# Kernel tuning notes

Hardware: AMD Instinct MI355X
Metric: run time of the kernel (lower is better)

## Reference

```python
import jax, jax.numpy as jnp
import numpy as np

NUM_HEADS = 32
NUM_KV_HEADS = 8
HEAD_DIM = 128
WINDOW = 512
NUM_META = 4


def _swa_sink_mask(S):
    # allowed = causal & (within sliding window OR sink/meta token)
    i = jnp.arange(S)[:, None]   # q_idx
    j = jnp.arange(S)[None, :]   # kv_idx
    return (i >= j) & (((i - j) <= WINDOW) | (j < NUM_META))


def setup_inputs() -> dict:
    key = jax.random.key(0)
    k1, k2, k3 = jax.random.split(key, 3)
    B, S = 1, 2048
    return {
        "query_states": jax.random.normal(k1, (B, S, NUM_HEADS * HEAD_DIM), dtype=jnp.float32),
        "key_states": jax.random.normal(k2, (B, S, NUM_KV_HEADS * HEAD_DIM), dtype=jnp.float32),
        "value_states": jax.random.normal(k3, (B, S, NUM_KV_HEADS * HEAD_DIM), dtype=jnp.float32),
    }


def reference(query_states, key_states, value_states):
    B, S, _ = query_states.shape
    n_rep = NUM_HEADS // NUM_KV_HEADS
    # [B, H, S, D]
    q = query_states.reshape(B, S, NUM_HEADS, HEAD_DIM).transpose(0, 2, 1, 3)
    k = key_states.reshape(B, S, NUM_KV_HEADS, HEAD_DIM).transpose(0, 2, 1, 3)
    v = value_states.reshape(B, S, NUM_KV_HEADS, HEAD_DIM).transpose(0, 2, 1, 3)
    # repeat_kv: interleaved repeat along head dim (GQA)
    k = jnp.repeat(k, n_rep, axis=1)
    v = jnp.repeat(v, n_rep, axis=1)

    scale = 1.0 / jnp.sqrt(jnp.float32(HEAD_DIM))  # flex_attention default scale
    scores = jnp.einsum("bhqd,bhkd->bhqk", q, k) * scale
    mask = _swa_sink_mask(S)  # [S, S], every row has q_idx==kv_idx allowed
    scores = jnp.where(mask[None, None], scores, -jnp.inf)
    attn = jax.nn.softmax(scores, axis=-1)
    out = jnp.einsum("bhqk,bhkd->bhqd", attn, v)
    return out.transpose(0, 2, 1, 3).reshape(B, S, NUM_HEADS * HEAD_DIM)
```

## Files before the change

### kernel.cpp

```cpp
#include <hip/hip_runtime.h>
#include <math.h>

typedef __attribute__((ext_vector_type(8))) short bf16x8;
typedef __attribute__((ext_vector_type(16))) float f32x16;

#define WIN 512
#define META 4
#define KSTR 136
#define VSTR 72
#define PSTRD 36
#define QSCALE 0.08838834764831845f
#define MFIX 14.0f

union U8 { int4 i4; bf16x8 bf; };

__device__ __forceinline__ unsigned bf16_rne(float x) {
  unsigned u = __float_as_uint(x);
  return (u + 0x7FFFu + ((u >> 16) & 1u)) >> 16;
}
__device__ __forceinline__ unsigned pk2_rne(float a, float b) {
  return bf16_rne(a) | (bf16_rne(b) << 16);
}
__device__ __forceinline__ unsigned pk2_tr(float a, float b) {
  return (__float_as_uint(a) >> 16) | (__float_as_uint(b) & 0xFFFF0000u);
}

__global__ __launch_bounds__(256, 2) void swa_fused(
    const float* __restrict__ Qg, const float* __restrict__ Kg,
    const float* __restrict__ Vg, float* __restrict__ Og)
{
  __shared__ __align__(16) unsigned short Ks[64 * KSTR];
  __shared__ __align__(16) unsigned short Vts[128 * VSTR];
  __shared__ __align__(16) unsigned Pw[4 * 32 * PSTRD];

  const int tid = threadIdx.x;
  const int lane = tid & 63, wid = tid >> 6;
  const int cl = lane & 31, hl = lane >> 5;
  const int hk = blockIdx.y;
  const int h  = hk * 4 + wid;
  const int bx = blockIdx.x;
  const int qtile = (bx & 1) ? (63 - (bx >> 1)) : (bx >> 1);
  const int q0 = qtile * 32;

  const int sh = tid >> 5;
  const int sc = (tid & 31) * 4;
  const int kq = tid >> 4;
  const int dg = tid & 15;
  const int vchi = ((kq >> 1) ^ (dg & 7)) * 8 + (kq & 1) * 4;

  int4 qf[8];
  {
    const float* qrow = Qg + (size_t)(q0 + cl) * 4096 + h * 128 + hl * 8;
    #pragma unroll
    for (int kc = 0; kc < 8; ++kc) {
      float4 x = *(const float4*)(qrow + kc * 16);
      float4 y = *(const float4*)(qrow + kc * 16 + 4);
      qf[kc] = make_int4(pk2_rne(x.x*QSCALE, x.y*QSCALE), pk2_rne(x.z*QSCALE, x.w*QSCALE),
                         pk2_rne(y.x*QSCALE, y.y*QSCALE), pk2_rne(y.z*QSCALE, y.w*QSCALE));
    }
  }

  f32x16 acc[4];
  #pragma unroll
  for (int nt = 0; nt < 4; ++nt)
    #pragma unroll
    for (int i = 0; i < 16; ++i) acc[nt][i] = 0.f;
  float lp[16];
  #pragma unroll
  for (int i = 0; i < 16; ++i) lp[i] = 0.f;

  unsigned* PwW = Pw + wid * 32 * PSTRD;

  const int jstart = (q0 > WIN) ? ((q0 - WIN) & ~63) : 0;
  const int sink = (jstart > 0) ? 1 : 0;
  const int niter = ((q0 + 31 - jstart) >> 6) + 1 + sink;

  float4 kreg[8], vreg[8];
  {
    const int jt0 = sink ? 0 : jstart;
    const float* kb = Kg + (size_t)jt0 * 1024 + hk * 128 + sc;
    #pragma unroll
    for (int it = 0; it < 8; ++it)
      kreg[it] = *(const float4*)(kb + (size_t)(it * 8 + sh) * 1024);
    const float* vb = Vg + (size_t)jt0 * 1024 + hk * 128 + dg * 8;
    #pragma unroll
    for (int r = 0; r < 4; ++r) {
      const int row = ((r & 1) ? 1 : 0) + ((r >> 1) ? 32 : 0) + 2 * kq;
      vreg[2*r]   = *(const float4*)(vb + (size_t)row * 1024);
      vreg[2*r+1] = *(const float4*)(vb + (size_t)row * 1024 + 4);
    }
  }

  for (int t = 0; t < niter; ++t) {
    const bool isSink = (sink != 0) && (t == 0);
    const int jt = isSink ? 0 : jstart + ((t - sink) << 6);
    const bool needMask = (jt + 63 > q0) || (q0 + 31 - jt > WIN);

    __syncthreads();

    #pragma unroll
    for (int it = 0; it < 8; ++it) {
      float4 v = kreg[it];
      *(uint2*)(Ks + (it * 8 + sh) * KSTR + sc) =
          make_uint2(pk2_tr(v.x, v.y), pk2_tr(v.z, v.w));
    }
    #pragma unroll
    for (int half = 0; half < 2; ++half) {
      const float* p0 = (const float*)&vreg[half];
      const float* p1 = (const float*)&vreg[2 + half];
      const float* p2 = (const float*)&vreg[4 + half];
      const float* p3 = (const float*)&vreg[6 + half];
      #pragma unroll
      for (int e = 0; e < 4; ++e) {
        const int dp = dg * 8 + half * 4 + e;
        *(uint2*)(Vts + dp * VSTR + vchi) =
            make_uint2(pk2_tr(p0[e], p2[e]), pk2_tr(p1[e], p3[e]));
      }
    }
    __syncthreads();

    if (t + 1 < niter) {
      const int jn = jstart + ((t + 1 - sink) << 6);
      const float* kb = Kg + (size_t)jn * 1024 + hk * 128 + sc;
      #pragma unroll
      for (int it = 0; it < 8; ++it)
        kreg[it] = *(const float4*)(kb + (size_t)(it * 8 + sh) * 1024);
      const float* vb = Vg + (size_t)jn * 1024 + hk * 128 + dg * 8;
      #pragma unroll
      for (int r = 0; r < 4; ++r) {
        const int row = ((r & 1) ? 1 : 0) + ((r >> 1) ? 32 : 0) + 2 * kq;
        vreg[2*r]   = *(const float4*)(vb + (size_t)row * 1024);
        vreg[2*r+1] = *(const float4*)(vb + (size_t)row * 1024 + 4);
      }
    }

    f32x16 s0v, s1v;
    #pragma unroll
    for (int i = 0; i < 16; ++i) { s0v[i] = 0.f; s1v[i] = 0.f; }
    #pragma unroll
    for (int kc = 0; kc < 8; ++kc) {
      U8 a; a.i4 = qf[kc];
      U8 b0; b0.i4 = *(const int4*)(Ks + cl * KSTR + kc * 16 + hl * 8);
      s0v = __builtin_amdgcn_mfma_f32_32x32x16_bf16(a.bf, b0.bf, s0v, 0, 0, 0);
      U8 b1; b1.i4 = *(const int4*)(Ks + (32 + cl) * KSTR + kc * 16 + hl * 8);
      s1v = __builtin_amdgcn_mfma_f32_32x32x16_bf16(a.bf, b1.bf, s1v, 0, 0, 0);
    }

    const int k0 = jt + cl, k1 = jt + 32 + cl;
    #pragma unroll
    for (int ri = 0; ri < 16; ++ri) {
      const int rl = (ri & 3) + 8 * (ri >> 2) + 4 * hl;
      float sa = s0v[ri] - MFIX;
      float sb = s1v[ri] - MFIX;
      if (needMask) {
        const int row = q0 + rl;
        const int d0 = row - k0, d1 = row - k1;
        if (!((d0 >= 0) && ((d0 <= WIN) || (k0 < META)))) sa = -1e30f;
        if (!((d1 >= 0) && ((d1 <= WIN) || (k1 < META)))) sb = -1e30f;
      }
      float p0 = __expf(sa), p1 = __expf(sb);
      unsigned u0 = __float_as_uint(p0) & 0xFFFF0000u;
      unsigned u1 = __float_as_uint(p1) & 0xFFFF0000u;
      lp[ri] += __uint_as_float(u0) + __uint_as_float(u1);
      PwW[rl * PSTRD + cl] = (u0 >> 16) | u1;
    }

    const int kcmax = isSink ? 1 : 4;
    for (int kc = 0; kc < kcmax; ++kc) {
      U8 a; a.i4 = *(const int4*)(PwW + cl * PSTRD + kc * 8 + hl * 4);
      #pragma unroll
      for (int nt = 0; nt < 4; ++nt) {
        const int dim = nt * 32 + cl;
        const int chi = ((2 * kc + hl) ^ ((dim >> 3) & 7)) * 8;
        U8 b; b.i4 = *(const int4*)(Vts + dim * VSTR + chi);
        acc[nt] = __builtin_amdgcn_mfma_f32_32x32x16_bf16(a.bf, b.bf, acc[nt], 0, 0, 0);
      }
    }
  }

  #pragma unroll
  for (int ri = 0; ri < 16; ++ri) {
    float v = lp[ri];
    v += __shfl_xor(v, 1);  v += __shfl_xor(v, 2);  v += __shfl_xor(v, 4);
    v += __shfl_xor(v, 8);  v += __shfl_xor(v, 16);
    lp[ri] = __fdividef(1.0f, v);
  }
  #pragma unroll
  for (int nt = 0; nt < 4; ++nt) {
    #pragma unroll
    for (int ri = 0; ri < 16; ++ri) {
      const int rl = (ri & 3) + 8 * (ri >> 2) + 4 * hl;
      Og[(size_t)(q0 + rl) * 4096 + h * 128 + nt * 32 + cl] = acc[nt][ri] * lp[ri];
    }
  }
}

extern "C" void kernel_launch(void* const* d_in, const int* in_sizes, int n_in,
                              void* d_out, int out_size, void* d_ws, size_t ws_size,
                              hipStream_t stream) {
  const float* Q = (const float*)d_in[0];
  const float* K = (const float*)d_in[1];
  const float* V = (const float*)d_in[2];
  float* O = (float*)d_out;
  hipLaunchKernelGGL(swa_fused, dim3(64, 8), dim3(256), 0, stream, Q, K, V, O);
}
```

Baseline: 132.9 us.

## Compute transposed scores so P stays in registers, dropping LDS round trip

Swaps MFMA operands so the score tile is K-by-Q, which lets each lane pack its exponentiated probabilities directly into the A operand for the PV MFMA instead of writing them to shared memory and reading them back. The V staging layout in LDS is reordered to match the new key ordering, and the row-sum becomes a per-lane scalar reduced with one cross-half shuffle. The sink tile skips its second QK MFMA, and the grid is flattened to 1D with KV heads interleaved so neighbouring blocks share a query tile. The cost is more register pressure from the pu0/pu1 arrays, plus an extra shuffle per output row in the epilogue.

Measured after the change: 123.9 us. 6.8% less time.

```diff
diff --git a/kernel.cpp b/kernel.cpp
--- a/kernel.cpp
+++ b/kernel.cpp
@@ -8,20 +8,19 @@
 #define META 4
 #define KSTR 136
 #define VSTR 72
-#define PSTRD 36
 #define QSCALE 0.08838834764831845f
 #define MFIX 14.0f
 
 union U8 { int4 i4; bf16x8 bf; };
 
-__device__ __forceinline__ unsigned bf16_rne(float x) {
+static __device__ __forceinline__ unsigned bf16_rne(float x) {
   unsigned u = __float_as_uint(x);
   return (u + 0x7FFFu + ((u >> 16) & 1u)) >> 16;
 }
-__device__ __forceinline__ unsigned pk2_rne(float a, float b) {
+static __device__ __forceinline__ unsigned pk2_rne(float a, float b) {
   return bf16_rne(a) | (bf16_rne(b) << 16);
 }
-__device__ __forceinline__ unsigned pk2_tr(float a, float b) {
+static __device__ __forceinline__ unsigned pk2_tr(float a, float b) {
   return (__float_as_uint(a) >> 16) | (__float_as_uint(b) & 0xFFFF0000u);
 }
 
@@ -31,22 +30,23 @@
 {
   __shared__ __align__(16) unsigned short Ks[64 * KSTR];
   __shared__ __align__(16) unsigned short Vts[128 * VSTR];
-  __shared__ __align__(16) unsigned Pw[4 * 32 * PSTRD];
 
   const int tid = threadIdx.x;
   const int lane = tid & 63, wid = tid >> 6;
   const int cl = lane & 31, hl = lane >> 5;
-  const int hk = blockIdx.y;
-  const int h  = hk * 4 + wid;
-  const int bx = blockIdx.x;
-  const int qtile = (bx & 1) ? (63 - (bx >> 1)) : (bx >> 1);
+  const int bid = blockIdx.x;
+  const int hk = bid & 7;
+  const int bq = bid >> 3;
+  const int qtile = (bq & 1) ? (63 - (bq >> 1)) : (bq >> 1);
   const int q0 = qtile * 32;
+  const int h = hk * 4 + wid;
 
   const int sh = tid >> 5;
   const int sc = (tid & 31) * 4;
+  const int dg = tid & 15;
   const int kq = tid >> 4;
-  const int dg = tid & 15;
-  const int vchi = ((kq >> 1) ^ (dg & 7)) * 8 + (kq & 1) * 4;
+  const int vchunk = 2 * (kq >> 2) + (kq & 1);
+  const int vhalf  = (kq >> 1) & 1;
 
   int4 qf[8];
   {
@@ -65,11 +65,7 @@
   for (int nt = 0; nt < 4; ++nt)
     #pragma unroll
     for (int i = 0; i < 16; ++i) acc[nt][i] = 0.f;
-  float lp[16];
-  #pragma unroll
-  for (int i = 0; i < 16; ++i) lp[i] = 0.f;
-
-  unsigned* PwW = Pw + wid * 32 * PSTRD;
+  float lp = 0.f;
 
   const int jstart = (q0 > WIN) ? ((q0 - WIN) & ~63) : 0;
   const int sink = (jstart > 0) ? 1 : 0;
@@ -84,10 +80,9 @@
       kreg[it] = *(const float4*)(kb + (size_t)(it * 8 + sh) * 1024);
     const float* vb = Vg + (size_t)jt0 * 1024 + hk * 128 + dg * 8;
     #pragma unroll
-    for (int r = 0; r < 4; ++r) {
-      const int row = ((r & 1) ? 1 : 0) + ((r >> 1) ? 32 : 0) + 2 * kq;
-      vreg[2*r]   = *(const float4*)(vb + (size_t)row * 1024);
-      vreg[2*r+1] = *(const float4*)(vb + (size_t)row * 1024 + 4);
+    for (int i = 0; i < 4; ++i) {
+      vreg[2*i]   = *(const float4*)(vb + (size_t)(4 * kq + i) * 1024);
+      vreg[2*i+1] = *(const float4*)(vb + (size_t)(4 * kq + i) * 1024 + 4);
     }
   }
 
@@ -105,17 +100,15 @@
           make_uint2(pk2_tr(v.x, v.y), pk2_tr(v.z, v.w));
     }
     #pragma unroll
-    for (int half = 0; half < 2; ++half) {
-      const float* p0 = (const float*)&vreg[half];
-      const float* p1 = (const float*)&vreg[2 + half];
-      const float* p2 = (const float*)&vreg[4 + half];
-      const float* p3 = (const float*)&vreg[6 + half];
-      #pragma unroll
-      for (int e = 0; e < 4; ++e) {
-        const int dp = dg * 8 + half * 4 + e;
-        *(uint2*)(Vts + dp * VSTR + vchi) =
-            make_uint2(pk2_tr(p0[e], p2[e]), pk2_tr(p1[e], p3[e]));
-      }
+    for (int e = 0; e < 8; ++e) {
+      const int d = dg * 8 + e;
+      const int half = e >> 2, c = e & 3;
+      const float* f0 = (const float*)&vreg[0 + half];
+      const float* f1 = (const float*)&vreg[2 + half];
+      const float* f2 = (const float*)&vreg[4 + half];
+      const float* f3 = (const float*)&vreg[6 + half];
+      *(uint2*)(Vts + d * VSTR + ((vchunk ^ (dg & 7)) << 3) + (vhalf << 2)) =
+          make_uint2(pk2_tr(f0[c], f1[c]), pk2_tr(f2[c], f3[c]));
     }
     __syncthreads();
 
@@ -127,70 +120,80 @@
         kreg[it] = *(const float4*)(kb + (size_t)(it * 8 + sh) * 1024);
       const float* vb = Vg + (size_t)jn * 1024 + hk * 128 + dg * 8;
       #pragma unroll
-      for (int r = 0; r < 4; ++r) {
-        const int row = ((r & 1) ? 1 : 0) + ((r >> 1) ? 32 : 0) + 2 * kq;
-        vreg[2*r]   = *(const float4*)(vb + (size_t)row * 1024);
-        vreg[2*r+1] = *(const float4*)(vb + (size_t)row * 1024 + 4);
+      for (int i = 0; i < 4; ++i) {
+        vreg[2*i]   = *(const float4*)(vb + (size_t)(4 * kq + i) * 1024);
+        vreg[2*i+1] = *(const float4*)(vb + (size_t)(4 * kq + i) * 1024 + 4);
       }
     }
 
     f32x16 s0v, s1v;
     #pragma unroll
     for (int i = 0; i < 16; ++i) { s0v[i] = 0.f; s1v[i] = 0.f; }
-    #pragma unroll
-    for (int kc = 0; kc < 8; ++kc) {
-      U8 a; a.i4 = qf[kc];
-      U8 b0; b0.i4 = *(const int4*)(Ks + cl * KSTR + kc * 16 + hl * 8);
-      s0v = __builtin_amdgcn_mfma_f32_32x32x16_bf16(a.bf, b0.bf, s0v, 0, 0, 0);
-      U8 b1; b1.i4 = *(const int4*)(Ks + (32 + cl) * KSTR + kc * 16 + hl * 8);
-      s1v = __builtin_amdgcn_mfma_f32_32x32x16_bf16(a.bf, b1.bf, s1v, 0, 0, 0);
-    }
-
-    const int k0 = jt + cl, k1 = jt + 32 + cl;
+    if (isSink) {
+      #pragma unroll
+      for (int kc = 0; kc < 8; ++kc) {
+        U8 b; b.i4 = qf[kc];
+        U8 a0; a0.i4 = *(const int4*)(Ks + cl * KSTR + kc * 16 + hl * 8);
+        s0v = __builtin_amdgcn_mfma_f32_32x32x16_bf16(a0.bf, b.bf, s0v, 0, 0, 0);
+      }
+    } else {
+      #pragma unroll
+      for (int kc = 0; kc < 8; ++kc) {
+        U8 b; b.i4 = qf[kc];
+        U8 a0; a0.i4 = *(const int4*)(Ks + cl * KSTR + kc * 16 + hl * 8);
+        s0v = __builtin_amdgcn_mfma_f32_32x32x16_bf16(a0.bf, b.bf, s0v, 0, 0, 0);
+        U8 a1; a1.i4 = *(const int4*)(Ks + (32 + cl) * KSTR + kc * 16 + hl * 8);
+        s1v = __builtin_amdgcn_mfma_f32_32x32x16_bf16(a1.bf, b.bf, s1v, 0, 0, 0);
+      }
+    }
+
+    unsigned pu0[16], pu1[16];
+    const int q = q0 + cl;
     #pragma unroll
     for (int ri = 0; ri < 16; ++ri) {
-      const int rl = (ri & 3) + 8 * (ri >> 2) + 4 * hl;
-      float sa = s0v[ri] - MFIX;
-      float sb = s1v[ri] - MFIX;
+      const int koff = (ri & 3) + 8 * (ri >> 2) + 4 * hl;
+      bool ok0 = true, ok1 = true;
       if (needMask) {
-        const int row = q0 + rl;
-        const int d0 = row - k0, d1 = row - k1;
-        if (!((d0 >= 0) && ((d0 <= WIN) || (k0 < META)))) sa = -1e30f;
-        if (!((d1 >= 0) && ((d1 <= WIN) || (k1 < META)))) sb = -1e30f;
-      }
-      float p0 = __expf(sa), p1 = __expf(sb);
-      unsigned u0 = __float_as_uint(p0) & 0xFFFF0000u;
-      unsigned u1 = __float_as_uint(p1) & 0xFFFF0000u;
-      lp[ri] += __uint_as_float(u0) + __uint_as_float(u1);
-      PwW[rl * PSTRD + cl] = (u0 >> 16) | u1;
-    }
-
+        const int k0v = jt + koff, k1v = jt + 32 + koff;
+        ok0 = (q >= k0v) && (((q - k0v) <= WIN) || (k0v < META));
+        ok1 = (q >= k1v) && (((q - k1v) <= WIN) || (k1v < META));
+      }
+      unsigned u0 = ok0 ? (__float_as_uint(__expf(s0v[ri] - MFIX)) & 0xFFFF0000u) : 0u;
+      pu0[ri] = u0;
+      lp += __uint_as_float(u0);
+      if (!isSink) {
+        unsigned u1 = ok1 ? (__float_as_uint(__expf(s1v[ri] - MFIX)) & 0xFFFF0000u) : 0u;
+        pu1[ri] = u1;
+        lp += __uint_as_float(u1);
+      }
+    }
+
+    #define MKA(P, o) make_int4((P[(o)] >> 16) | P[(o)+1], (P[(o)+2] >> 16) | P[(o)+3], \
+                                (P[(o)+4] >> 16) | P[(o)+5], (P[(o)+6] >> 16) | P[(o)+7])
     const int kcmax = isSink ? 1 : 4;
     for (int kc = 0; kc < kcmax; ++kc) {
-      U8 a; a.i4 = *(const int4*)(PwW + cl * PSTRD + kc * 8 + hl * 4);
+      U8 a;
+      a.i4 = (kc == 0) ? MKA(pu0, 0) : (kc == 1) ? MKA(pu0, 8)
+           : (kc == 2) ? MKA(pu1, 0) : MKA(pu1, 8);
       #pragma unroll
       for (int nt = 0; nt < 4; ++nt) {
         const int dim = nt * 32 + cl;
-        const int chi = ((2 * kc + hl) ^ ((dim >> 3) & 7)) * 8;
-        U8 b; b.i4 = *(const int4*)(Vts + dim * VSTR + chi);
+        U8 b; b.i4 = *(const int4*)(Vts + dim * VSTR + (((2 * kc + hl) ^ ((dim >> 3) & 7)) << 3));
         acc[nt] = __builtin_amdgcn_mfma_f32_32x32x16_bf16(a.bf, b.bf, acc[nt], 0, 0, 0);
       }
     }
-  }
-
+    #undef MKA
+  }
+
+  const float ltot = lp + __shfl_xor(lp, 32);
+  const float inv = __fdividef(1.0f, ltot);
   #pragma unroll
   for (int ri = 0; ri < 16; ++ri) {
-    float v = lp[ri];
-    v += __shfl_xor(v, 1);  v += __shfl_xor(v, 2);  v += __shfl_xor(v, 4);
-    v += __shfl_xor(v, 8);  v += __shfl_xor(v, 16);
-    lp[ri] = __fdividef(1.0f, v);
-  }
-  #pragma unroll
-  for (int nt = 0; nt < 4; ++nt) {
-    #pragma unroll
-    for (int ri = 0; ri < 16; ++ri) {
-      const int rl = (ri & 3) + 8 * (ri >> 2) + 4 * hl;
-      Og[(size_t)(q0 + rl) * 4096 + h * 128 + nt * 32 + cl] = acc[nt][ri] * lp[ri];
+    const int rl = (ri & 3) + 8 * (ri >> 2) + 4 * hl;
+    const float invq = __shfl(inv, rl, 64);
+    #pragma unroll
+    for (int nt = 0; nt < 4; ++nt) {
+      Og[(size_t)(q0 + rl) * 4096 + h * 128 + nt * 32 + cl] = acc[nt][ri] * invq;
     }
   }
 }
@@ -202,5 +205,5 @@
   const float* K = (const float*)d_in[1];
   const float* V = (const float*)d_in[2];
   float* O = (float*)d_out;
-  hipLaunchKernelGGL(swa_fused, dim3(64, 8), dim3(256), 0, stream, Q, K, V, O);
-}
+  hipLaunchKernelGGL(swa_fused, dim3(512), dim3(256), 0, stream, Q, K, V, O);
+}
```
